# Kernel optimization log

Hardware: AMD Instinct MI355X
Metric: run time of the kernel (lower is better)

Reference implementation:

```python
import jax, jax.numpy as jnp
import numpy as np

N, M_DIM, CTRL = 16384, 512, 1024
EPS = 1e-16

def setup_inputs() -> dict:
    key = jax.random.key(0)
    k1, k2, k3, k4, k5 = jax.random.split(key, 5)
    embeddings = jax.random.normal(k1, (1, CTRL), dtype=jnp.float32)
    w_prev = jax.random.uniform(k2, (1, N), dtype=jnp.float32)
    w_prev = w_prev / jnp.sum(w_prev, axis=1, keepdims=True)  # valid soft address
    memory = jax.random.normal(k3, (N, M_DIM), dtype=jnp.float32) * 0.05
    out_f = 3 * M_DIM + 6  # write_lengths = [M,1,1,3,1,M,M]
    W = jax.random.normal(k4, (out_f, CTRL), dtype=jnp.float32) * (1.0 / np.sqrt(CTRL))
    b = jax.random.normal(k5, (out_f,), dtype=jnp.float32) * 0.01
    return {"embeddings": embeddings, "w_prev": w_prev, "memory": memory, "W": W, "b": b}

def reference(embeddings, w_prev, memory, W, b):
    Md = memory.shape[1]
    o = (embeddings @ W.T + b).reshape(1, -1)  # [1, 3M+6]
    # column split per write_lengths [M,1,1,3,1,M,M]
    k = o[:, :Md]
    beta = jax.nn.softplus(o[:, Md:Md + 1])
    g = jax.nn.sigmoid(o[:, Md + 1:Md + 2])
    s = jax.nn.softmax(o[:, Md + 2:Md + 5], axis=1)       # 3 circular shifts
    gamma = 1.0 + jax.nn.softplus(o[:, Md + 5:Md + 6])
    e = o[:, Md + 6:2 * Md + 6]                            # erase vector [1,M]
    a = o[:, 2 * Md + 6:]                                  # add vector   [1,M]
    # content addressing: cosine similarity of k against each memory row
    mem_norm = jnp.linalg.norm(memory, axis=1)             # [N]
    k_norm = jnp.linalg.norm(k, axis=1)                    # [1]
    sim = (k @ memory.T) / (k_norm[:, None] * mem_norm[None, :] + EPS)  # [1,N]
    wc = jax.nn.softmax(beta * sim, axis=1)
    # interpolation with previous weights
    wg = g * wc + (1.0 - g) * w_prev
    # circular convolution with 3-tap shift kernel (shifts -1,0,+1)
    ws = (s[:, 0:1] * jnp.roll(wg, 1, axis=1)
          + s[:, 1:2] * wg
          + s[:, 2:3] * jnp.roll(wg, -1, axis=1))
    # sharpening
    wp = jnp.power(ws + EPS, gamma)
    w = wp / jnp.sum(wp, axis=1, keepdims=True)            # [1,N]
    # erase/add outer-product memory write
    erase = w.T @ e                                        # [N,M]
    add = w.T @ a                                          # [N,M]
    new_memory = memory * (1.0 - erase) + add
    return w, new_memory
```

## Files before the change

### kernel.cpp

```cpp
#include <hip/hip_runtime.h>
#include <math.h>

#define N 16384
#define MD 512
#define CTRLDIM 1024
#define OUTF 1542


__device__ __forceinline__ float softplus_f(float x) {
    return (x > 20.f) ? x : log1pf(expf(x));
}

__device__ __forceinline__ float wave_bfly_sum(float v) {
    #pragma unroll
    for (int off = 1; off < 64; off <<= 1) v += __shfl_xor(v, off, 64);
    return v;
}

__global__ void k_proj(const float* __restrict__ emb, const float* __restrict__ W,
                       const float* __restrict__ b, float* __restrict__ O,
                       float* __restrict__ E, float* __restrict__ A) {
    int row = blockIdx.x;
    int t = threadIdx.x;
    const float4* w4 = (const float4*)(W + (size_t)row * CTRLDIM);
    const float4* e4 = (const float4*)emb;
    float4 wv = w4[t];
    float4 ev = e4[t];
    float p = wv.x * ev.x + wv.y * ev.y + wv.z * ev.z + wv.w * ev.w;
    #pragma unroll
    for (int off = 32; off; off >>= 1) p += __shfl_down(p, off, 64);
    __shared__ float s[4];
    int lane = t & 63, wid = t >> 6;
    if (lane == 0) s[wid] = p;
    __syncthreads();
    if (t == 0) {
        float val = s[0] + s[1] + s[2] + s[3] + b[row];
        O[row] = val;
        if (row >= MD + 6 && row < 2 * MD + 6)      E[row - (MD + 6)] = val;
        else if (row >= 2 * MD + 6)                 A[row - (2 * MD + 6)] = val;
    }
}

__global__ void __launch_bounds__(256) k_sim(const float* __restrict__ mem,
                                             const float* __restrict__ O,
                                             float* __restrict__ EZ,
                                             float* __restrict__ PART1) {
    int t = threadIdx.x, lane = t & 63, wid = t >> 6;
    int waveId = blockIdx.x * 4 + wid;
    const float4* k4 = (const float4*)O;
    float4 k0 = k4[lane], k1 = k4[lane + 64];
    float ksq = k0.x * k0.x + k0.y * k0.y + k0.z * k0.z + k0.w * k0.w
              + k1.x * k1.x + k1.y * k1.y + k1.z * k1.z + k1.w * k1.w;
    ksq = wave_bfly_sum(ksq);
    float knorm = sqrtf(ksq);
    float beta = softplus_f(O[MD]);
    int row0 = waveId * 4;
    float4 m0[4], m1[4];
    #pragma unroll
    for (int r = 0; r < 4; r++) {
        const float4* m4 = (const float4*)(mem + (size_t)(row0 + r) * MD);
        m0[r] = m4[lane];
        m1[r] = m4[lane + 64];
    }
    float wsum = 0.f;
    #pragma unroll
    for (int r = 0; r < 4; r++) {
        float dot = m0[r].x * k0.x + m0[r].y * k0.y + m0[r].z * k0.z + m0[r].w * k0.w
                  + m1[r].x * k1.x + m1[r].y * k1.y + m1[r].z * k1.z + m1[r].w * k1.w;
        float nsq = m0[r].x * m0[r].x + m0[r].y * m0[r].y + m0[r].z * m0[r].z + m0[r].w * m0[r].w
                  + m1[r].x * m1[r].x + m1[r].y * m1[r].y + m1[r].z * m1[r].z + m1[r].w * m1[r].w;
        dot = wave_bfly_sum(dot);
        nsq = wave_bfly_sum(nsq);
        float z = beta * dot / (knorm * sqrtf(nsq) + 1e-16f);
        float ez = expf(z - beta);
        if (lane == 0) EZ[row0 + r] = ez;
        wsum += ez;
    }
    __shared__ float sblk[4];
    if (lane == 0) sblk[wid] = wsum;
    __syncthreads();
    if (t == 0) PART1[blockIdx.x] = sblk[0] + sblk[1] + sblk[2] + sblk[3];
}

__global__ void __launch_bounds__(256) k_shift(const float* __restrict__ EZ,
                                               const float* __restrict__ wprev,
                                               const float* __restrict__ O,
                                               const float* __restrict__ PART1,
                                               float* __restrict__ WP,
                                               float* __restrict__ PART2) {
    int t = threadIdx.x, lane = t & 63, wid = t >> 6;
    float v = 0.f;
    #pragma unroll
    for (int j = 0; j < 16; j++) v += PART1[lane + j * 64];
    float inv1 = 1.f / wave_bfly_sum(v);
    float g = 1.f / (1.f + expf(-O[MD + 1]));
    float s0r = O[MD + 2], s1r = O[MD + 3], s2r = O[MD + 4];
    float m = fmaxf(s0r, fmaxf(s1r, s2r));
    float e0 = expf(s0r - m), e1 = expf(s1r - m), e2 = expf(s2r - m);
    float inv_se = 1.f / (e0 + e1 + e2);
    float s0 = e0 * inv_se, s1 = e1 * inv_se, s2 = e2 * inv_se;
    float gamma = 1.f + softplus_f(O[MD + 5]);
    float gm1 = 1.f - g;
    int i = blockIdx.x * 256 + t;
    int im = (i == 0) ? (N - 1) : (i - 1);
    int ip = (i == N - 1) ? 0 : (i + 1);
    float wgm = g * EZ[im] * inv1 + gm1 * wprev[im];
    float wgc = g * EZ[i]  * inv1 + gm1 * wprev[i];
    float wgp = g * EZ[ip] * inv1 + gm1 * wprev[ip];
    float wsv = s0 * wgm + s1 * wgc + s2 * wgp;
    float wp = exp2f(gamma * log2f(wsv + 1e-16f));
    WP[i] = wp;
    float bs = wave_bfly_sum(wp);
    __shared__ float sblk[4];
    if (lane == 0) sblk[wid] = bs;
    __syncthreads();
    if (t == 0) PART2[blockIdx.x] = sblk[0] + sblk[1] + sblk[2] + sblk[3];
}

__global__ void __launch_bounds__(256) k_upd(const float* __restrict__ mem,
                                             const float* __restrict__ WP,
                                             const float* __restrict__ PART2,
                                             const float* __restrict__ E,
                                             const float* __restrict__ A,
                                             float* __restrict__ wout,
                                             float* __restrict__ outMem) {
    int t = threadIdx.x, lane = t & 63;
    float inv2 = 1.f / wave_bfly_sum(PART2[lane]);
    int idx = blockIdx.x * 256 + t;
    int i = idx >> 7;
    int c = idx & 127;
    float wi = WP[i] * inv2;
    if (c == 0) wout[i] = wi;
    float4 m = ((const float4*)mem)[idx];
    float4 e = ((const float4*)E)[c];
    float4 a = ((const float4*)A)[c];
    float4 o;
    o.x = m.x * (1.f - wi * e.x) + wi * a.x;
    o.y = m.y * (1.f - wi * e.y) + wi * a.y;
    o.z = m.z * (1.f - wi * e.z) + wi * a.z;
    o.w = m.w * (1.f - wi * e.w) + wi * a.w;
    ((float4*)outMem)[idx] = o;
}

extern "C" void kernel_launch(void* const* d_in, const int* in_sizes, int n_in,
                              void* d_out, int out_size, void* d_ws, size_t ws_size,
                              hipStream_t stream) {
    const float* emb   = (const float*)d_in[0];
    const float* wprev = (const float*)d_in[1];
    const float* mem   = (const float*)d_in[2];
    const float* W     = (const float*)d_in[3];
    const float* b     = (const float*)d_in[4];
    float* out = (float*)d_out;
    float* wsf = (float*)d_ws;
    float* O     = wsf;
    float* E     = wsf + 1552;
    float* A     = wsf + 2064;
    float* PART1 = wsf + 2576;
    float* PART2 = wsf + 3600;
    float* EZ    = wsf + 3664;
    float* WP    = wsf + 20048;

    k_proj<<<OUTF, 256, 0, stream>>>(emb, W, b, O, E, A);
    k_sim<<<N / 16, 256, 0, stream>>>(mem, O, EZ, PART1);
    k_shift<<<N / 256, 256, 0, stream>>>(EZ, wprev, O, PART1, WP, PART2);
    k_upd<<<(N * (MD / 4)) / 256, 256, 0, stream>>>(mem, WP, PART2, E, A, out, out + N);
}
```

Before: 109.6 us.

## Fuse similarity, shift and memory update into one cooperative kernel

Replaces the three post-projection kernels with a single cooperative-groups kernel that uses grid-wide syncs between the similarity, shift/sharpen and update phases. Each block keeps its 16 memory rows in LDS (32 KB), so the update phase writes new memory without re-reading it from global memory, and two kernel launch boundaries are removed. In exchange it adds two grid barriers, needs all 1024 blocks co-resident (4 per CU at 32 KB LDS each), and keeps the old path as a fallback when cooperative launch is unavailable or fails.

```diff
diff --git a/kernel.cpp b/kernel.cpp
--- a/kernel.cpp
+++ b/kernel.cpp
@@ -1,10 +1,13 @@
 #include <hip/hip_runtime.h>
+#include <hip/hip_cooperative_groups.h>
 #include <math.h>
 
 #define N 16384
 #define MD 512
 #define CTRLDIM 1024
 #define OUTF 1542
+
+namespace cg = cooperative_groups;
 
 
 __device__ __forceinline__ float softplus_f(float x) {
@@ -38,6 +41,110 @@
         O[row] = val;
         if (row >= MD + 6 && row < 2 * MD + 6)      E[row - (MD + 6)] = val;
         else if (row >= 2 * MD + 6)                 A[row - (2 * MD + 6)] = val;
+    }
+}
+
+__global__ void __launch_bounds__(256, 4) k_fused(
+        const float* __restrict__ mem, const float* __restrict__ O,
+        const float* __restrict__ wprev, const float* __restrict__ E,
+        const float* __restrict__ A, float* __restrict__ EZ,
+        float* __restrict__ PART1, float* __restrict__ PART2,
+        float* __restrict__ wout, float* __restrict__ outMem) {
+    __shared__ float4 smem[2048];
+    __shared__ float wp_s[16];
+    __shared__ float sred[4];
+
+    int t = threadIdx.x, lane = t & 63, wid = t >> 6;
+    int b = blockIdx.x;
+
+    const float4* k4 = (const float4*)O;
+    float4 kk0 = k4[lane], kk1 = k4[lane + 64];
+    float ksq = kk0.x * kk0.x + kk0.y * kk0.y + kk0.z * kk0.z + kk0.w * kk0.w
+              + kk1.x * kk1.x + kk1.y * kk1.y + kk1.z * kk1.z + kk1.w * kk1.w;
+    ksq = wave_bfly_sum(ksq);
+    float knorm = sqrtf(ksq);
+    float beta = softplus_f(O[MD]);
+    int row0 = (b * 4 + wid) * 4;
+    float4 m0[4], m1[4];
+    #pragma unroll
+    for (int r = 0; r < 4; r++) {
+        const float4* m4 = (const float4*)(mem + (size_t)(row0 + r) * MD);
+        m0[r] = m4[lane];
+        m1[r] = m4[lane + 64];
+    }
+    float wsum = 0.f;
+    #pragma unroll
+    for (int r = 0; r < 4; r++) {
+        smem[(wid * 4 + r) * 128 + lane]      = m0[r];
+        smem[(wid * 4 + r) * 128 + 64 + lane] = m1[r];
+        float dot = m0[r].x * kk0.x + m0[r].y * kk0.y + m0[r].z * kk0.z + m0[r].w * kk0.w
+                  + m1[r].x * kk1.x + m1[r].y * kk1.y + m1[r].z * kk1.z + m1[r].w * kk1.w;
+        float nsq = m0[r].x * m0[r].x + m0[r].y * m0[r].y + m0[r].z * m0[r].z + m0[r].w * m0[r].w
+                  + m1[r].x * m1[r].x + m1[r].y * m1[r].y + m1[r].z * m1[r].z + m1[r].w * m1[r].w;
+        dot = wave_bfly_sum(dot);
+        nsq = wave_bfly_sum(nsq);
+        float z = beta * dot / (knorm * sqrtf(nsq) + 1e-16f);
+        float ez = expf(z - beta);
+        if (lane == 0) EZ[row0 + r] = ez;
+        wsum += ez;
+    }
+    if (lane == 0) sred[wid] = wsum;
+    __syncthreads();
+    if (t == 0) PART1[b] = sred[0] + sred[1] + sred[2] + sred[3];
+
+    cg::this_grid().sync();
+
+    if (wid == 0) {
+        float v = 0.f;
+        #pragma unroll
+        for (int j = 0; j < 16; j++) v += PART1[lane + j * 64];
+        float inv1 = 1.f / wave_bfly_sum(v);
+        float g = 1.f / (1.f + expf(-O[MD + 1]));
+        float s0r = O[MD + 2], s1r = O[MD + 3], s2r = O[MD + 4];
+        float mx = fmaxf(s0r, fmaxf(s1r, s2r));
+        float e0 = expf(s0r - mx), e1 = expf(s1r - mx), e2 = expf(s2r - mx);
+        float inv_se = 1.f / (e0 + e1 + e2);
+        float s0 = e0 * inv_se, s1 = e1 * inv_se, s2 = e2 * inv_se;
+        float gamma = 1.f + softplus_f(O[MD + 5]);
+        float gm1 = 1.f - g;
+        int r = lane & 15;
+        int i = b * 16 + r;
+        int im = (i == 0) ? (N - 1) : (i - 1);
+        int ip = (i == N - 1) ? 0 : (i + 1);
+        float wgm = g * EZ[im] * inv1 + gm1 * wprev[im];
+        float wgc = g * EZ[i]  * inv1 + gm1 * wprev[i];
+        float wgp = g * EZ[ip] * inv1 + gm1 * wprev[ip];
+        float wsv = s0 * wgm + s1 * wgc + s2 * wgp;
+        float wp = exp2f(gamma * log2f(wsv + 1e-16f));
+        if (lane < 16) wp_s[r] = wp;
+        float bs = wave_bfly_sum((lane < 16) ? wp : 0.f);
+        if (lane == 0) PART2[b] = bs;
+    }
+
+    cg::this_grid().sync();
+
+    float v2 = 0.f;
+    #pragma unroll
+    for (int j = 0; j < 16; j++) v2 += PART2[lane + j * 64];
+    float inv2 = 1.f / wave_bfly_sum(v2);
+    if (t < 16) wout[b * 16 + t] = wp_s[t] * inv2;
+    const float4* E4 = (const float4*)E;
+    const float4* A4 = (const float4*)A;
+    float4* out4 = (float4*)outMem;
+    #pragma unroll
+    for (int q = 0; q < 8; q++) {
+        int idx = t + q * 256;
+        int rl = idx >> 7, c = idx & 127;
+        float wi = wp_s[rl] * inv2;
+        float4 mv = smem[idx];
+        float4 e = E4[c];
+        float4 a = A4[c];
+        float4 o;
+        o.x = mv.x * (1.f - wi * e.x) + wi * a.x;
+        o.y = mv.y * (1.f - wi * e.y) + wi * a.y;
+        o.z = mv.z * (1.f - wi * e.z) + wi * a.z;
+        o.w = mv.w * (1.f - wi * e.w) + wi * a.w;
+        out4[(size_t)b * 2048 + idx] = o;
     }
 }
 
@@ -157,11 +264,34 @@
     float* A     = wsf + 2064;
     float* PART1 = wsf + 2576;
     float* PART2 = wsf + 3600;
-    float* EZ    = wsf + 3664;
-    float* WP    = wsf + 20048;
+    float* EZ    = wsf + 4624;
+    float* WP    = wsf + 21008;
 
     k_proj<<<OUTF, 256, 0, stream>>>(emb, W, b, O, E, A);
-    k_sim<<<N / 16, 256, 0, stream>>>(mem, O, EZ, PART1);
-    k_shift<<<N / 256, 256, 0, stream>>>(EZ, wprev, O, PART1, WP, PART2);
-    k_upd<<<(N * (MD / 4)) / 256, 256, 0, stream>>>(mem, WP, PART2, E, A, out, out + N);
-}
+
+    static int coop = -1;
+    if (coop < 0) {
+        int dev = 0, val = 0;
+        hipGetDevice(&dev);
+        hipDeviceGetAttribute(&val, hipDeviceAttributeCooperativeLaunch, dev);
+        coop = val;
+    }
+
+    bool done = false;
+    if (coop) {
+        const float* memp = mem;  const float* Op = O;  const float* wprevp = wprev;
+        const float* Ep = E;      const float* Ap = A;
+        float* EZp = EZ; float* P1p = PART1; float* P2p = PART2;
+        float* woutp = out; float* outMemp = out + N;
+        void* args[] = {(void*)&memp, (void*)&Op, (void*)&wprevp, (void*)&Ep, (void*)&Ap,
+                        (void*)&EZp, (void*)&P1p, (void*)&P2p, (void*)&woutp, (void*)&outMemp};
+        hipError_t err = hipLaunchCooperativeKernel((const void*)k_fused,
+                                                    dim3(1024), dim3(256), args, 0, stream);
+        done = (err == hipSuccess);
+    }
+    if (!done) {
+        k_sim<<<N / 16, 256, 0, stream>>>(mem, O, EZ, PART1);
+        k_shift<<<N / 256, 256, 0, stream>>>(EZ, wprev, O, PART1, WP, PART2);
+        k_upd<<<(N * (MD / 4)) / 256, 256, 0, stream>>>(mem, WP, PART2, E, A, out, out + N);
+    }
+}
```

New measurement: 280.8 us. 2.56x slower.
